# Kernel tuning notes

Measured on AMD Instinct MI355X. Metric: run time of the kernel, lower is better.

The kernel has to match this reference:

```python
import jax, jax.numpy as jnp
import numpy as np

SHIFT = 1  # shift_direction fixed to +1 (original picks +/-1 randomly at init)


def setup_inputs() -> dict:
    key = jax.random.key(0)
    kx, kw = jax.random.split(key)
    x = jax.random.normal(kx, (128, 128, 56, 56), dtype=jnp.float32)  # (N, C, H, W)
    w = jax.random.normal(kw, (32, 3, 128), dtype=jnp.float32)        # (out_ch, ktap, in_ch)
    return {"x": x, "w": w}


def reference(x, w):
    # roll along W (original dim 3), then 1x3 conv along W with SAME padding,
    # then roll the output along H (original dim 2).
    xr = jnp.roll(x, SHIFT, axis=3)
    # einsum 'nkmilo,jki->njmlo' == correlation: y[n,j,h,w] = sum_{k,i} xr[n,i,h,w+k-1] * w[j,k,i]
    kernel = jnp.transpose(w, (0, 2, 1))[:, :, None, :]  # (O=32, I=128, kh=1, kw=3)
    y = jax.lax.conv_general_dilated(
        xr, kernel,
        window_strides=(1, 1),
        padding=((0, 0), (1, 1)),
        dimension_numbers=("NCHW", "OIHW", "NCHW"),
    )  # (128, 32, 56, 56)
    return jnp.roll(y, SHIFT, axis=2)
```

## Files before the change

### kernel.cpp

```cpp
#include <hip/hip_runtime.h>
#include <stddef.h>


#define C_IN   128
#define C_OUT  32
#define HH     56
#define WW     56
#define HW     3136
#define KTOT   384
#define WSTRIDE 392
#define XSTRIDE 136

typedef short bf16x8 __attribute__((ext_vector_type(8)));
typedef float f32x4  __attribute__((ext_vector_type(4)));

static __device__ __forceinline__ unsigned short f2b(float f) {
    unsigned u = __builtin_bit_cast(unsigned, f);
    unsigned r = u + 0x7FFFu + ((u >> 16) & 1u);
    return (unsigned short)(r >> 16);
}

__global__ void pack_w_kernel(const float* __restrict__ w, unsigned short* __restrict__ ws) {
    int idx = blockIdx.x * 256 + threadIdx.x;
    if (idx < C_OUT * WSTRIDE) {
        int j = idx / WSTRIDE;
        int r = idx % WSTRIDE;
        float v = (r < KTOT) ? w[j * KTOT + r] : 0.0f;
        ws[idx] = f2b(v);
    }
}

__global__ __launch_bounds__(256, 6)
void conv_mfma_kernel(const float* __restrict__ x, const unsigned short* __restrict__ ws,
                      float* __restrict__ out) {
    const int bid = blockIdx.x;
    const int n = bid / HH;
    const int h = bid % HH;
    const int hp = (h + HH - 1) % HH;

    const int tid  = threadIdx.x;
    const int lane = tid & 63;
    const int grp  = tid >> 6;

    __shared__ __align__(16) unsigned short XT[57 * XSTRIDE];

    {
        const int c = lane;
        const int i0 = grp * 32;
        if (c < WW) {
            const float* xp = x + (size_t)n * (C_IN * HW) + (size_t)i0 * HW + hp * WW + c;
            float v[32];
#pragma unroll
            for (int s = 0; s < 32; ++s) v[s] = xp[(size_t)s * HW];
            unsigned pk[16];
#pragma unroll
            for (int s = 0; s < 16; ++s)
                pk[s] = (unsigned)f2b(v[2 * s]) | ((unsigned)f2b(v[2 * s + 1]) << 16);
            uint4* dst = (uint4*)&XT[c * XSTRIDE + i0];
#pragma unroll
            for (int q = 0; q < 4; ++q)
                dst[q] = make_uint4(pk[4 * q], pk[4 * q + 1], pk[4 * q + 2], pk[4 * q + 3]);
        } else if (c == WW) {
            uint4* dst = (uint4*)&XT[WW * XSTRIDE + i0];
#pragma unroll
            for (int q = 0; q < 4; ++q) dst[q] = make_uint4(0, 0, 0, 0);
        }
    }
    __syncthreads();

    const int n0 = grp * 16;
    const int nn = n0 + (lane & 15);
    const int kb = (lane >> 4) * 8;

    int cc0 = (nn >= 1 && nn <= 55) ? (nn + 54) % WW : WW;
    int cc1 = (nn <= 55) ? (nn + 55) % WW : WW;
    int cc2 = (nn <= 54) ? nn : WW;
    const unsigned short* bp0 = &XT[cc0 * XSTRIDE + kb];
    const unsigned short* bp1 = &XT[cc1 * XSTRIDE + kb];
    const unsigned short* bp2 = &XT[cc2 * XSTRIDE + kb];

    const unsigned short* wp = ws + (lane & 15) * WSTRIDE + kb;

    f32x4 acc0 = {0.f, 0.f, 0.f, 0.f};
    f32x4 acc1 = {0.f, 0.f, 0.f, 0.f};

#pragma unroll
    for (int c = 0; c < 12; ++c) {
        const int tap = c >> 2;
        const int ib = (c & 3) * 32;
        const unsigned short* bp = (tap == 0) ? bp0 : (tap == 1) ? bp1 : bp2;
        bf16x8 b  = *(const bf16x8*)(bp + ib);
        bf16x8 a0 = *(const bf16x8*)(wp + c * 32);
        bf16x8 a1 = *(const bf16x8*)(wp + 16 * WSTRIDE + c * 32);
        acc0 = __builtin_amdgcn_mfma_f32_16x16x32_bf16(a0, b, acc0, 0, 0, 0);
        acc1 = __builtin_amdgcn_mfma_f32_16x16x32_bf16(a1, b, acc1, 0, 0, 0);
    }

    if (nn < WW) {
        float* ob = out + (size_t)n * (C_OUT * HW) + (size_t)h * WW + nn;
        const int j0 = (lane >> 4) * 4;
#pragma unroll
        for (int r = 0; r < 4; ++r) {
            ob[(size_t)(j0 + r) * HW]      = acc0[r];
            ob[(size_t)(j0 + r + 16) * HW] = acc1[r];
        }
    }
}

extern "C" void kernel_launch(void* const* d_in, const int* in_sizes, int n_in,
                              void* d_out, int out_size, void* d_ws, size_t ws_size,
                              hipStream_t stream) {
    const float* x = (const float*)d_in[0];
    const float* w = (const float*)d_in[1];
    float* out = (float*)d_out;
    unsigned short* ws = (unsigned short*)d_ws;

    pack_w_kernel<<<(C_OUT * WSTRIDE + 255) / 256, 256, 0, stream>>>(w, ws);
    conv_mfma_kernel<<<dim3(128 * HH), dim3(256), 0, stream>>>(x, ws, out);
}
```

Measured before the change: 325.5 us.

## Process two output rows per block and load input with float4 reads

Each block now computes two consecutive output rows, so every weight fragment loaded from global memory feeds four MFMAs instead of two and the grid is halved. The input staging changes from per-thread strided scalar loads to coalesced float4 loads along W, with scattered 16-bit stores into the transposed LDS tile. LDS use doubles and the occupancy hint drops from 6 to 5. The scattered 2-byte LDS writes may cause bank conflicts.

```diff
diff --git a/kernel.cpp b/kernel.cpp
--- a/kernel.cpp
+++ b/kernel.cpp
@@ -10,6 +10,7 @@
 #define KTOT   384
 #define WSTRIDE 392
 #define XSTRIDE 136
+#define XROW   (57 * XSTRIDE)
 
 typedef short bf16x8 __attribute__((ext_vector_type(8)));
 typedef float f32x4  __attribute__((ext_vector_type(4)));
@@ -25,84 +26,85 @@
     if (idx < C_OUT * WSTRIDE) {
         int j = idx / WSTRIDE;
         int r = idx % WSTRIDE;
-        float v = (r < KTOT) ? w[j * KTOT + r] : 0.0f;
-        ws[idx] = f2b(v);
+        ws[idx] = f2b(r < KTOT ? w[j * KTOT + r] : 0.0f);
     }
 }
 
-__global__ __launch_bounds__(256, 6)
+__global__ __launch_bounds__(256, 5)
 void conv_mfma_kernel(const float* __restrict__ x, const unsigned short* __restrict__ ws,
                       float* __restrict__ out) {
-    const int bid = blockIdx.x;
-    const int n = bid / HH;
-    const int h = bid % HH;
-    const int hp = (h + HH - 1) % HH;
-
+    const int bid  = blockIdx.x;
+    const int n    = bid / (HH / 2);
+    const int h0   = (bid % (HH / 2)) * 2;
     const int tid  = threadIdx.x;
     const int lane = tid & 63;
     const int grp  = tid >> 6;
 
-    __shared__ __align__(16) unsigned short XT[57 * XSTRIDE];
+    __shared__ __align__(16) unsigned short XT[2 * XROW];
 
-    {
-        const int c = lane;
-        const int i0 = grp * 32;
-        if (c < WW) {
-            const float* xp = x + (size_t)n * (C_IN * HW) + (size_t)i0 * HW + hp * WW + c;
-            float v[32];
+    if (tid < 32) {
+        int r = tid >> 4, seg = tid & 15;
+        *(uint4*)&XT[r * XROW + WW * XSTRIDE + seg * 8] = make_uint4(0, 0, 0, 0);
+    }
+
+    const int hp0 = (h0 + HH - 1) % HH;
+    const float* xb = x + (size_t)n * (C_IN * HW);
+
 #pragma unroll
-            for (int s = 0; s < 32; ++s) v[s] = xp[(size_t)s * HW];
-            unsigned pk[16];
-#pragma unroll
-            for (int s = 0; s < 16; ++s)
-                pk[s] = (unsigned)f2b(v[2 * s]) | ((unsigned)f2b(v[2 * s + 1]) << 16);
-            uint4* dst = (uint4*)&XT[c * XSTRIDE + i0];
-#pragma unroll
-            for (int q = 0; q < 4; ++q)
-                dst[q] = make_uint4(pk[4 * q], pk[4 * q + 1], pk[4 * q + 2], pk[4 * q + 3]);
-        } else if (c == WW) {
-            uint4* dst = (uint4*)&XT[WW * XSTRIDE + i0];
-#pragma unroll
-            for (int q = 0; q < 4; ++q) dst[q] = make_uint4(0, 0, 0, 0);
-        }
+    for (int p = 0; p < 14; ++p) {
+        const int task = p * 256 + tid;
+        const int ch   = task & 127;
+        const int rest = task >> 7;
+        const int c4   = rest % 14;
+        const int r    = rest / 14;
+        const int hrow = (r == 0) ? hp0 : h0;
+        const float4 v = *(const float4*)(xb + (size_t)ch * HW + hrow * WW + c4 * 4);
+        unsigned short* dst = &XT[r * XROW + (c4 * 4) * XSTRIDE + ch];
+        dst[0]           = f2b(v.x);
+        dst[XSTRIDE]     = f2b(v.y);
+        dst[2 * XSTRIDE] = f2b(v.z);
+        dst[3 * XSTRIDE] = f2b(v.w);
     }
     __syncthreads();
 
-    const int n0 = grp * 16;
-    const int nn = n0 + (lane & 15);
+    const int nn = grp * 16 + (lane & 15);
     const int kb = (lane >> 4) * 8;
-
-    int cc0 = (nn >= 1 && nn <= 55) ? (nn + 54) % WW : WW;
-    int cc1 = (nn <= 55) ? (nn + 55) % WW : WW;
-    int cc2 = (nn <= 54) ? nn : WW;
-    const unsigned short* bp0 = &XT[cc0 * XSTRIDE + kb];
-    const unsigned short* bp1 = &XT[cc1 * XSTRIDE + kb];
-    const unsigned short* bp2 = &XT[cc2 * XSTRIDE + kb];
+    const int cc0 = (nn >= 1 && nn <= 55) ? (nn + 54) % WW : WW;
+    const int cc1 = (nn <= 55) ? (nn + 55) % WW : WW;
+    const int cc2 = (nn <= 54) ? nn : WW;
+    const unsigned short* b00 = &XT[cc0 * XSTRIDE + kb];
+    const unsigned short* b01 = &XT[cc1 * XSTRIDE + kb];
+    const unsigned short* b02 = &XT[cc2 * XSTRIDE + kb];
 
     const unsigned short* wp = ws + (lane & 15) * WSTRIDE + kb;
 
-    f32x4 acc0 = {0.f, 0.f, 0.f, 0.f};
-    f32x4 acc1 = {0.f, 0.f, 0.f, 0.f};
+    f32x4 acc00 = {0.f,0.f,0.f,0.f}, acc01 = {0.f,0.f,0.f,0.f};
+    f32x4 acc10 = {0.f,0.f,0.f,0.f}, acc11 = {0.f,0.f,0.f,0.f};
 
 #pragma unroll
     for (int c = 0; c < 12; ++c) {
         const int tap = c >> 2;
-        const int ib = (c & 3) * 32;
-        const unsigned short* bp = (tap == 0) ? bp0 : (tap == 1) ? bp1 : bp2;
-        bf16x8 b  = *(const bf16x8*)(bp + ib);
-        bf16x8 a0 = *(const bf16x8*)(wp + c * 32);
-        bf16x8 a1 = *(const bf16x8*)(wp + 16 * WSTRIDE + c * 32);
-        acc0 = __builtin_amdgcn_mfma_f32_16x16x32_bf16(a0, b, acc0, 0, 0, 0);
-        acc1 = __builtin_amdgcn_mfma_f32_16x16x32_bf16(a1, b, acc1, 0, 0, 0);
+        const int ib  = (c & 3) * 32;
+        const unsigned short* bp = (tap == 0) ? b00 : (tap == 1) ? b01 : b02;
+        bf16x8 A0 = *(const bf16x8*)(wp + c * 32);
+        bf16x8 A1 = *(const bf16x8*)(wp + 16 * WSTRIDE + c * 32);
+        bf16x8 B0 = *(const bf16x8*)(bp + ib);
+        bf16x8 B1 = *(const bf16x8*)(bp + XROW + ib);
+        acc00 = __builtin_amdgcn_mfma_f32_16x16x32_bf16(A0, B0, acc00, 0, 0, 0);
+        acc01 = __builtin_amdgcn_mfma_f32_16x16x32_bf16(A1, B0, acc01, 0, 0, 0);
+        acc10 = __builtin_amdgcn_mfma_f32_16x16x32_bf16(A0, B1, acc10, 0, 0, 0);
+        acc11 = __builtin_amdgcn_mfma_f32_16x16x32_bf16(A1, B1, acc11, 0, 0, 0);
     }
 
     if (nn < WW) {
-        float* ob = out + (size_t)n * (C_OUT * HW) + (size_t)h * WW + nn;
         const int j0 = (lane >> 4) * 4;
+        float* ob = out + (size_t)n * (C_OUT * HW) + (size_t)h0 * WW + nn;
 #pragma unroll
         for (int r = 0; r < 4; ++r) {
-            ob[(size_t)(j0 + r) * HW]      = acc0[r];
-            ob[(size_t)(j0 + r + 16) * HW] = acc1[r];
+            ob[(size_t)(j0 + r) * HW]           = acc00[r];
+            ob[(size_t)(j0 + r + 16) * HW]      = acc01[r];
+            ob[(size_t)(j0 + r) * HW + WW]      = acc10[r];
+            ob[(size_t)(j0 + r + 16) * HW + WW] = acc11[r];
         }
     }
 }
@@ -116,5 +118,5 @@
     unsigned short* ws = (unsigned short*)d_ws;
 
     pack_w_kernel<<<(C_OUT * WSTRIDE + 255) / 256, 256, 0, stream>>>(w, ws);
-    conv_mfma_kernel<<<dim3(128 * HH), dim3(256), 0, stream>>>(x, ws, out);
+    conv_mfma_kernel<<<dim3(128 * (HH / 2)), dim3(256), 0, stream>>>(x, ws, out);
 }
```

Measured after the change: 322.5 us. Within noise of the previous version (-0.9%).
